# Kernel optimization log

Hardware: AMD Instinct MI355X
Metric: run time of the kernel (lower is better)

The kernel has to match this reference:

```python
import jax, jax.numpy as jnp
import numpy as np

B, S, HID = 1, 2048, 4096
NH, NKV = 32, 8
HD = HID // NH            # 128
GROUPS = NH // NKV        # 4
ROPE_THETA = 10000.0


def _rope_cos_sin(seq_len, head_dim, dtype=jnp.float32):
    inv_freq = 1.0 / (ROPE_THETA ** (jnp.arange(0, head_dim, 2, dtype=jnp.float32) / head_dim))
    t = jnp.arange(seq_len, dtype=jnp.float32)
    freqs = jnp.outer(t, inv_freq)                      # [S, HD/2]
    emb = jnp.concatenate([freqs, freqs], axis=-1)      # [S, HD]
    return jnp.cos(emb).astype(dtype), jnp.sin(emb).astype(dtype)


def _rotate_half(x):
    x1, x2 = jnp.split(x, 2, axis=-1)
    return jnp.concatenate([-x2, x1], axis=-1)


def _apply_rope(x, cos, sin):
    # x: [B, H, S, HD]; cos/sin: [S, HD] (position_ids = arange(S), no past)
    return x * cos[None, None] + _rotate_half(x) * sin[None, None]


def setup_inputs() -> dict:
    key = jax.random.key(0)
    k1, k2, k3, k4, k5 = jax.random.split(key, 5)
    return {
        "hidden_states": jax.random.normal(k1, (B, S, HID), jnp.float32),
        "Wq": jax.random.normal(k2, (NH * HD, HID), jnp.float32) * 0.02,
        "Wk": jax.random.normal(k3, (NKV * HD, HID), jnp.float32) * 0.02,
        "Wv": jax.random.normal(k4, (NKV * HD, HID), jnp.float32) * 0.02,
        "Wo": jax.random.normal(k5, (HID, NH * HD), jnp.float32) * 0.02,
    }


def reference(hidden_states, Wq, Wk, Wv, Wo):
    bsz, q_len, _ = hidden_states.shape
    # projections (nn.Linear: x @ W.T)
    q = (hidden_states @ Wq.T).reshape(bsz, q_len, NH, HD).transpose(0, 2, 1, 3)   # [B,NH,S,HD]
    k = (hidden_states @ Wk.T).reshape(bsz, q_len, NKV, HD).transpose(0, 2, 1, 3)  # [B,NKV,S,HD]
    v = (hidden_states @ Wv.T).reshape(bsz, q_len, NKV, HD).transpose(0, 2, 1, 3)

    cos, sin = _rope_cos_sin(q_len, HD, hidden_states.dtype)
    q = _apply_rope(q, cos, sin)
    k = _apply_rope(k, cos, sin)

    # GQA: repeat kv heads (repeat_kv / num_key_value_groups)
    k = jnp.repeat(k, GROUPS, axis=1)   # [B,NH,S,HD]
    v = jnp.repeat(v, GROUPS, axis=1)

    scale = 1.0 / jnp.sqrt(jnp.asarray(HD, hidden_states.dtype))
    logits = jnp.einsum('bhqd,bhkd->bhqk', q, k) * scale   # [B,NH,S,S]

    # prefill causal mask (phys_past_len = 0)
    causal = jnp.tril(jnp.ones((q_len, q_len), dtype=bool))
    logits = jnp.where(causal[None, None], logits, jnp.finfo(logits.dtype).min)

    attn = jax.nn.softmax(logits, axis=-1)
    out = jnp.einsum('bhqk,bhkd->bhqd', attn, v)            # [B,NH,S,HD]
    out = out.transpose(0, 2, 1, 3).reshape(bsz, q_len, NH * HD)
    return out @ Wo.T
```

## Files before the change

### kernel.cpp

```cpp
#include <hip/hip_runtime.h>

typedef __bf16 bf16;
typedef __bf16 bf16x2 __attribute__((ext_vector_type(2)));
typedef __bf16 bf16x4 __attribute__((ext_vector_type(4)));
typedef __bf16 bf16x8 __attribute__((ext_vector_type(8)));
typedef float f32x4 __attribute__((ext_vector_type(4)));

#define S_LEN 2048
#define HID_DIM 4096
#define NH 32
#define NKV 8
#define HD 128
#define QKV_N 6144
#define K_COL 4096
#define V_COL 5120
#define PADV 76

__global__ void cvt_all_kernel(const float* __restrict__ hs, const float* __restrict__ wq,
                               const float* __restrict__ wk, const float* __restrict__ wv,
                               const float* __restrict__ wo, bf16* __restrict__ hsb,
                               bf16* __restrict__ wqkvb, bf16* __restrict__ wob,
                               float* __restrict__ cost, float* __restrict__ sint) {
  long i = (long)blockIdx.x * blockDim.x + threadIdx.x;
  if (i >= 12582912) {
    int j = (int)(i - 12582912);
    int s = j >> 6, d = j & 63;
    float inv = expf(-0.14391156831212787f * (float)d);
    float ang = (float)s * inv;
    cost[j] = cosf(ang);
    sint[j] = sinf(ang);
    return;
  }
  const float* src; bf16* dst; long off;
  if (i < 2097152)      { src = hs; dst = hsb;                          off = i; }
  else if (i < 6291456) { src = wq; dst = wqkvb;                        off = i - 2097152; }
  else if (i < 7340032) { src = wk; dst = wqkvb + (long)4096 * 4096;    off = i - 6291456; }
  else if (i < 8388608) { src = wv; dst = wqkvb + (long)5120 * 4096;    off = i - 7340032; }
  else                  { src = wo; dst = wob;                          off = i - 8388608; }
  float4 v = reinterpret_cast<const float4*>(src)[off];
  bf16x4 o;
  o[0] = (bf16)v.x; o[1] = (bf16)v.y; o[2] = (bf16)v.z; o[3] = (bf16)v.w;
  reinterpret_cast<bf16x4*>(dst)[off] = o;
}

__global__ void rope_apply_kernel(bf16* __restrict__ qkv, const float* __restrict__ cost,
                                  const float* __restrict__ sint) {
  int idx = blockIdx.x * blockDim.x + threadIdx.x;
  int s = idx / 320;
  int c = idx - s * 320;
  int g = c >> 3, dc = (c & 7) * 8;
  long base = (long)s * QKV_N + g * 128 + dc;
  bf16x8 x1 = *reinterpret_cast<const bf16x8*>(qkv + base);
  bf16x8 x2 = *reinterpret_cast<const bf16x8*>(qkv + base + 64);
  const float* cp = cost + (s << 6) + dc;
  const float* sp = sint + (s << 6) + dc;
  float4 ca = *reinterpret_cast<const float4*>(cp);
  float4 cb = *reinterpret_cast<const float4*>(cp + 4);
  float4 sa = *reinterpret_cast<const float4*>(sp);
  float4 sb = *reinterpret_cast<const float4*>(sp + 4);
  float co[8] = {ca.x, ca.y, ca.z, ca.w, cb.x, cb.y, cb.z, cb.w};
  float sn[8] = {sa.x, sa.y, sa.z, sa.w, sb.x, sb.y, sb.z, sb.w};
  bf16x8 y1, y2;
#pragma unroll
  for (int e = 0; e < 8; ++e) {
    float a = (float)x1[e], b = (float)x2[e];
    y1[e] = (bf16)(a * co[e] - b * sn[e]);
    y2[e] = (bf16)(b * co[e] + a * sn[e]);
  }
  *reinterpret_cast<bf16x8*>(qkv + base)      = y1;
  *reinterpret_cast<bf16x8*>(qkv + base + 64) = y2;
}

#define STG8(buf, mat, kt, unit) {                                                       \
    const bf16* sp_ = (mat) ? Bp : Ap;                                                   \
    int row0_ = ((mat) ? n0 : m0) + (unit) * 64;                                         \
    int lb_ = (buf) * LBUF + (mat) * 16384 + (unit) * 4096;                              \
    int r_ = t >> 3, jl_ = t & 7, jg_ = jl_ ^ (r_ & 7);                                  \
    const bf16* src_ = sp_ + (long)(row0_ + r_) * K + (kt) * 64 + jg_ * 8;               \
    __builtin_amdgcn_global_load_lds((const __attribute__((address_space(1))) void*)src_,\
        (__attribute__((address_space(3))) void*)(L + lb_ + t * 8), 16, 0, 0); }

#define DSA2(buf, mh) {                                                                  \
    _Pragma("unroll") for (int ks_ = 0; ks_ < 2; ++ks_)                                  \
      _Pragma("unroll") for (int mf_ = 0; mf_ < 4; ++mf_) {                              \
        int R_ = wr * 128 + (mh) * 64 + mf_ * 16 + lm;                                   \
        aF[ks_][mf_] = *reinterpret_cast<const bf16x8*>(                                 \
            L + (buf) * LBUF + R_ * 64 + (((ks_ * 4 + lg) ^ (R_ & 7)) << 3));            \
      } }

#define DSBALL(buf) {                                                                    \
    _Pragma("unroll") for (int ks_ = 0; ks_ < 2; ++ks_)                                  \
      _Pragma("unroll") for (int nf_ = 0; nf_ < NB; ++nf_) {                             \
        int R_ = wc * (NB * 16) + nf_ * 16 + lm;                                         \
        bF[ks_][nf_] = *reinterpret_cast<const bf16x8*>(                                 \
            L + (buf) * LBUF + 16384 + R_ * 64 + (((ks_ * 4 + lg) ^ (R_ & 7)) << 3));    \
      } }

#define MM2(mh) {                                                                        \
    __builtin_amdgcn_s_setprio(1);                                                       \
    _Pragma("unroll") for (int mf_ = 0; mf_ < 4; ++mf_)                                  \
      _Pragma("unroll") for (int nf_ = 0; nf_ < NB; ++nf_)                               \
        _Pragma("unroll") for (int ks_ = 0; ks_ < 2; ++ks_)                              \
          acc[(mh) * 4 + mf_][nf_] = __builtin_amdgcn_mfma_f32_16x16x32_bf16(            \
              aF[ks_][mf_], bF[ks_][nf_], acc[(mh) * 4 + mf_][nf_], 0, 0, 0);            \
    __builtin_amdgcn_s_setprio(0); }

#define BAR() __builtin_amdgcn_s_barrier()
#define WVM(n) asm volatile("s_waitcnt vmcnt(%0)" :: "i"(n) : "memory")

template<int NB, typename OutT>
__global__ __launch_bounds__(512, 1) void gemm4p_kernel(
    const bf16* __restrict__ Ap, const bf16* __restrict__ Bp, OutT* __restrict__ C,
    int M, int N, int K) {
  constexpr int LBUF = 16384 + NB * 4096;
  __shared__ __align__(16) bf16 L[2 * LBUF];

  int nwg = gridDim.x * gridDim.y;
  int bid = blockIdx.y * gridDim.x + blockIdx.x;
  int cpx = nwg >> 3;
  int swz = (bid & 7) * cpx + (bid >> 3);
  int bxs = swz % gridDim.x, bys = swz / gridDim.x;
  const int n0 = bxs * (NB * 64), m0 = bys * 256;

  const int t = threadIdx.x;
  const int lane = t & 63, w = t >> 6;
  const int wr = w >> 2, wc = w & 3;
  const int lg = lane >> 4, lm = lane & 15;
  const int NT = K >> 6;

  f32x4 acc[8][NB] = {};
  bf16x8 aF[2][4], bF[2][NB];

  STG8(0, 0, 0, 0); STG8(0, 0, 0, 1); STG8(0, 0, 0, 2); STG8(0, 0, 0, 3);
  STG8(0, 1, 0, 0); if (NB > 1) STG8(0, 1, 0, 1); if (NB > 2) STG8(0, 1, 0, 2);
  STG8(1, 1, 1, 0); if (NB > 1) STG8(1, 1, 1, 1); if (NB > 2) STG8(1, 1, 1, 2);
  WVM(NB);
  BAR();

  for (int I = 0; I < (NT >> 1); ++I) {
    const int tt = 2 * I;
    const bool pf = (I < (NT >> 1) - 1);
    DSA2(0, 0); DSBALL(0);
    STG8(1, 0, tt + 1, 0); STG8(1, 0, tt + 1, 1);
    STG8(1, 0, tt + 1, 2); STG8(1, 0, tt + 1, 3);
    BAR(); MM2(0); BAR();
    DSA2(0, 1);
    if (pf) { STG8(0, 1, tt + 2, 0); if (NB > 1) STG8(0, 1, tt + 2, 1);
              if (NB > 2) STG8(0, 1, tt + 2, 2); }
    BAR(); MM2(1);
    if (pf) WVM(NB); else WVM(0);
    BAR();
    DSA2(1, 0); DSBALL(1);
    if (pf) { STG8(0, 0, tt + 2, 0); STG8(0, 0, tt + 2, 1);
              STG8(0, 0, tt + 2, 2); STG8(0, 0, tt + 2, 3); }
    BAR(); MM2(0); BAR();
    DSA2(1, 1);
    if (pf) { STG8(1, 1, tt + 3, 0); if (NB > 1) STG8(1, 1, tt + 3, 1);
              if (NB > 2) STG8(1, 1, tt + 3, 2); }
    BAR(); MM2(1);
    if (pf) WVM(NB); else WVM(0);
    BAR();
  }

#pragma unroll
  for (int am = 0; am < 8; ++am) {
    int row = m0 + wr * 128 + am * 16 + lg * 4;
#pragma unroll
    for (int nf = 0; nf < NB; ++nf) {
      int col = n0 + wc * (NB * 16) + nf * 16 + lm;
#pragma unroll
      for (int rr = 0; rr < 4; ++rr) {
        if constexpr (sizeof(OutT) == 4) C[(long)(row + rr) * N + col] = acc[am][nf][rr];
        else                             C[(long)(row + rr) * N + col] = (bf16)acc[am][nf][rr];
      }
    }
  }
}

#define AK_LBAR() { asm volatile("s_waitcnt lgkmcnt(0)" ::: "memory");                   \
                    __builtin_amdgcn_s_barrier(); }
#define AK_VBAR() { asm volatile("s_waitcnt vmcnt(4)" ::: "memory");                     \
                    __builtin_amdgcn_sched_barrier(0);                                   \
                    asm volatile("s_waitcnt lgkmcnt(0)" ::: "memory");                   \
                    __builtin_amdgcn_s_barrier(); }

#define AK_WRITEV(r0, r1) {                                                              \
    _Pragma("unroll") for (int e = 0; e < 8; ++e) {                                      \
      bf16x2 pk; pk[0] = r0[e]; pk[1] = r1[e];                                           \
      *reinterpret_cast<bf16x2*>(Vt + (dchunk * 8 + e) * PADV + slot) = pk;              \
    } }

#define AK_ISSUEV(base, r0, r1) {                                                        \
    long rv_ = (long)(base) + kva; if (rv_ > 2046) rv_ = 2046;                           \
    const bf16* vs_ = vbase + rv_ * QKV_N + dchunk * 8;                                  \
    r0 = *reinterpret_cast<const bf16x8*>(vs_);                                          \
    r1 = *reinterpret_cast<const bf16x8*>(vs_ + QKV_N); }

#define AK_ISSUEK(base, buf) {                                                           \
    _Pragma("unroll") for (int i_ = 0; i_ < 2; ++i_) {                                   \
      int c_ = i_ * 512 + t;                                                             \
      int r_ = c_ >> 4, jl_ = c_ & 15, jg_ = jl_ ^ (r_ & 15);                            \
      long rk_ = (long)(base) + r_; if (rk_ > 2047) rk_ = 2047;                          \
      const bf16* src_ = kbase + rk_ * QKV_N + jg_ * 8;                                  \
      __builtin_amdgcn_global_load_lds((const __attribute__((address_space(1))) void*)src_,\
          (__attribute__((address_space(3))) void*)(Ks[buf] + c_ * 8), 16, 0, 0);        \
    } }

#define AK_STEP(stv, ksb) {                                                              \
    const int st_ = (stv);                                                               \
    const int kv0_ = st_ * 64;                                                           \
    if (kv0_ <= q0 + w * 16 + 15) {                                                      \
      f32x4 s[4];                                                                        \
      _Pragma("unroll") for (int cb = 0; cb < 4; ++cb) s[cb] = f32x4{0.f,0.f,0.f,0.f};   \
      __builtin_amdgcn_s_setprio(1);                                                     \
      _Pragma("unroll") for (int ks = 0; ks < 4; ++ks)                                   \
        _Pragma("unroll") for (int cb = 0; cb < 4; ++cb) {                               \
          bf16x8 kf = *reinterpret_cast<const bf16x8*>(                                  \
              Ks[ksb] + (cb * 16 + lm) * 128 + (((ks * 4 + lg) ^ lm) << 3));             \
          s[cb] = __builtin_amdgcn_mfma_f32_16x16x32_bf16(kf, qf[ks], s[cb], 0, 0, 0);   \
        }                                                                                \
      __builtin_amdgcn_s_setprio(0);                                                     \
      const float SC = 0.12751742f;                                                      \
      float sl[4][4];                                                                    \
      _Pragma("unroll") for (int cb = 0; cb < 4; ++cb)                                   \
        _Pragma("unroll") for (int r = 0; r < 4; ++r) {                                  \
          float v = s[cb][r] * SC;                                                       \
          if (st_ >= nst - 2 && (kv0_ + cb * 16 + lg * 4 + r) > qg) v = -1e30f;          \
          sl[cb][r] = v;                                                                 \
        }                                                                                \
      float tm = sl[0][0];                                                               \
      _Pragma("unroll") for (int cb = 0; cb < 4; ++cb)                                   \
        _Pragma("unroll") for (int r = 0; r < 4; ++r) tm = fmaxf(tm, sl[cb][r]);         \
      tm = fmaxf(tm, __shfl_xor(tm, 16));                                                \
      tm = fmaxf(tm, __shfl_xor(tm, 32));                                                \
      if (__any(tm > mrow + 8.f)) {                                                      \
        float mnew = fmaxf(mrow, tm);                                                    \
        float alpha = exp2f(mrow - mnew);                                                \
        mrow = mnew; lrow *= alpha;                                                      \
        float ar[4];                                                                     \
        _Pragma("unroll") for (int r = 0; r < 4; ++r)                                    \
          ar[r] = __shfl(alpha, (lane & 48) | (lg * 4 + r));                             \
        _Pragma("unroll") for (int i = 0; i < 8; ++i)                                    \
          _Pragma("unroll") for (int r = 0; r < 4; ++r) o[i][r] *= ar[r];                \
      }                                                                                  \
      float p[4][4]; float psum = 0.f;                                                   \
      _Pragma("unroll") for (int cb = 0; cb < 4; ++cb)                                   \
        _Pragma("unroll") for (int r = 0; r < 4; ++r) {                                  \
          p[cb][r] = exp2f(sl[cb][r] - mrow); psum += p[cb][r];                          \
        }                                                                                \
      psum += __shfl_xor(psum, 16);                                                      \
      psum += __shfl_xor(psum, 32);                                                      \
      lrow += psum;                                                                      \
      bf16x8 pa0, pa1;                                                                   \
      _Pragma("unroll") for (int r = 0; r < 4; ++r) {                                    \
        pa0[r] = (bf16)p[0][r]; pa0[4 + r] = (bf16)p[1][r];                              \
        pa1[r] = (bf16)p[2][r]; pa1[4 + r] = (bf16)p[3][r];                              \
      }                                                                                  \
      __builtin_amdgcn_s_setprio(1);                                                     \
      _Pragma("unroll") for (int db = 0; db < 8; ++db) {                                 \
        bf16x8 vf0 = *reinterpret_cast<const bf16x8*>(Vt + (db*16+lm)*PADV + lg*8);      \
        bf16x8 vf1 = *reinterpret_cast<const bf16x8*>(Vt + (db*16+lm)*PADV + 32 + lg*8); \
        o[db] = __builtin_amdgcn_mfma_f32_16x16x32_bf16(pa0, vf0, o[db], 0, 0, 0);       \
        o[db] = __builtin_amdgcn_mfma_f32_16x16x32_bf16(pa1, vf1, o[db], 0, 0, 0);       \
      }                                                                                  \
      __builtin_amdgcn_s_setprio(0);                                                     \
    } }

__global__ __launch_bounds__(512, 4) void attn_kernel(const bf16* __restrict__ qkv,
                                                      bf16* __restrict__ out) {
  __shared__ __align__(16) bf16 Ks[2][64 * 128];
  __shared__ __align__(16) bf16 Vt[128 * PADV];

  const int bx = blockIdx.x;
  const int qt = 15 - (bx >> 5);
  const int h = bx & 31;
  const int kvh = h >> 2;
  const int q0 = qt * 128;
  const int t = threadIdx.x, lane = t & 63, w = t >> 6;
  const int lg = lane >> 4, lm = lane & 15;
  const int dchunk = t >> 5, kv2 = t & 31;
  const int kva = kv2 * 2;
  const int k5 = kva & 31;
  const int slot = ((kva >> 5) << 5) | (((k5 >> 2) & 3) << 3) | ((k5 >> 4) << 2) | (k5 & 3);
  const bf16* kbase = qkv + K_COL + kvh * HD;
  const bf16* vbase = qkv + V_COL + kvh * HD;

  const long qrow = q0 + w * 16 + lm;
  const int qg = q0 + w * 16 + lm;
  bf16x8 qf[4];
#pragma unroll
  for (int ks = 0; ks < 4; ++ks)
    qf[ks] = *reinterpret_cast<const bf16x8*>(qkv + qrow * QKV_N + h * HD + ks * 32 + lg * 8);

  f32x4 o[8];
#pragma unroll
  for (int i = 0; i < 8; ++i) o[i] = f32x4{0.f, 0.f, 0.f, 0.f};
  float mrow = -1e30f, lrow = 0.f;

  const int nst = 2 * qt + 2;
  bf16x8 va0, va1, vb0, vb1;

  AK_ISSUEV(0, va0, va1);
  AK_ISSUEK(0, 0);
  AK_ISSUEV(64, vb0, vb1);
  AK_ISSUEK(64, 1);
  AK_WRITEV(va0, va1);
  AK_VBAR();

  for (int I = 0; I < (nst >> 1); ++I) {
    const int s0 = 2 * I;
    AK_STEP(s0, 0);
    AK_LBAR();
    AK_WRITEV(vb0, vb1);
    AK_ISSUEV((s0 + 2) * 64, va0, va1);
    AK_ISSUEK((s0 + 2) * 64, 0);
    AK_VBAR();
    AK_STEP(s0 + 1, 1);
    AK_LBAR();
    AK_WRITEV(va0, va1);
    AK_ISSUEV((s0 + 3) * 64, vb0, vb1);
    AK_ISSUEK((s0 + 3) * 64, 1);
    AK_VBAR();
  }

  float invr[4];
#pragma unroll
  for (int r = 0; r < 4; ++r)
    invr[r] = 1.0f / __shfl(lrow, (lane & 48) | (lg * 4 + r));
#pragma unroll
  for (int r = 0; r < 4; ++r) {
    long row = q0 + w * 16 + lg * 4 + r;
#pragma unroll
    for (int db = 0; db < 8; ++db)
      out[row * HID_DIM + h * HD + db * 16 + lm] = (bf16)(o[db][r] * invr[r]);
  }
}

extern "C" void kernel_launch(void* const* d_in, const int* in_sizes, int n_in,
                              void* d_out, int out_size, void* d_ws, size_t ws_size,
                              hipStream_t stream) {
  const float* hs = (const float*)d_in[0];
  const float* Wq = (const float*)d_in[1];
  const float* Wk = (const float*)d_in[2];
  const float* Wv = (const float*)d_in[3];
  const float* Wo = (const float*)d_in[4];
  float* out = (float*)d_out;
  char* ws = (char*)d_ws;

  bf16*  hsb   = (bf16*)(ws);
  bf16*  wqkvb = (bf16*)(ws + 16777216);
  bf16*  wob   = (bf16*)(ws + 67108864);
  bf16*  qkv   = (bf16*)(ws + 100663296);
  bf16*  attn  = (bf16*)(ws + 125829120);
  float* cost  = (float*)(ws + 142606336);
  float* sint  = (float*)(ws + 143130624);

  cvt_all_kernel<<<49664, 256, 0, stream>>>(hs, Wq, Wk, Wv, Wo, hsb, wqkvb, wob, cost, sint);
  gemm4p_kernel<3, bf16><<<dim3(32, 8), 512, 0, stream>>>(hsb, wqkvb, qkv, 2048, 6144, 4096);
  rope_apply_kernel<<<2560, 256, 0, stream>>>(qkv, cost, sint);
  attn_kernel<<<512, 512, 0, stream>>>(qkv, attn);
  gemm4p_kernel<2, float><<<dim3(32, 8), 512, 0, stream>>>(attn, wob, out, 2048, 4096, 4096);
}
```

Baseline: 302.5 us.

## Halve GEMM M-tile for more workgroups; double-buffer V in attention pipeline

```diff
diff --git a/kernel.cpp b/kernel.cpp
--- a/kernel.cpp
+++ b/kernel.cpp
@@ -71,48 +71,48 @@
   *reinterpret_cast<bf16x8*>(qkv + base + 64) = y2;
 }
 
-#define STG8(buf, mat, kt, unit) {                                                       \
+#define SG(buf, mat, kt, unit) {                                                         \
     const bf16* sp_ = (mat) ? Bp : Ap;                                                   \
     int row0_ = ((mat) ? n0 : m0) + (unit) * 64;                                         \
-    int lb_ = (buf) * LBUF + (mat) * 16384 + (unit) * 4096;                              \
+    int lb_ = (buf) * LBUF + (mat) * 8192 + (unit) * 4096;                               \
     int r_ = t >> 3, jl_ = t & 7, jg_ = jl_ ^ (r_ & 7);                                  \
     const bf16* src_ = sp_ + (long)(row0_ + r_) * K + (kt) * 64 + jg_ * 8;               \
     __builtin_amdgcn_global_load_lds((const __attribute__((address_space(1))) void*)src_,\
         (__attribute__((address_space(3))) void*)(L + lb_ + t * 8), 16, 0, 0); }
 
-#define DSA2(buf, mh) {                                                                  \
+#define RA(buf, mh) {                                                                    \
     _Pragma("unroll") for (int ks_ = 0; ks_ < 2; ++ks_)                                  \
-      _Pragma("unroll") for (int mf_ = 0; mf_ < 4; ++mf_) {                              \
-        int R_ = wr * 128 + (mh) * 64 + mf_ * 16 + lm;                                   \
+      _Pragma("unroll") for (int mf_ = 0; mf_ < 2; ++mf_) {                              \
+        int R_ = wr * 64 + (mh) * 32 + mf_ * 16 + lm;                                    \
         aF[ks_][mf_] = *reinterpret_cast<const bf16x8*>(                                 \
             L + (buf) * LBUF + R_ * 64 + (((ks_ * 4 + lg) ^ (R_ & 7)) << 3));            \
       } }
 
-#define DSBALL(buf) {                                                                    \
+#define RB(buf) {                                                                        \
     _Pragma("unroll") for (int ks_ = 0; ks_ < 2; ++ks_)                                  \
       _Pragma("unroll") for (int nf_ = 0; nf_ < NB; ++nf_) {                             \
         int R_ = wc * (NB * 16) + nf_ * 16 + lm;                                         \
         bF[ks_][nf_] = *reinterpret_cast<const bf16x8*>(                                 \
-            L + (buf) * LBUF + 16384 + R_ * 64 + (((ks_ * 4 + lg) ^ (R_ & 7)) << 3));    \
+            L + (buf) * LBUF + 8192 + R_ * 64 + (((ks_ * 4 + lg) ^ (R_ & 7)) << 3));     \
       } }
 
-#define MM2(mh) {                                                                        \
+#define MMH(mh) {                                                                        \
     __builtin_amdgcn_s_setprio(1);                                                       \
-    _Pragma("unroll") for (int mf_ = 0; mf_ < 4; ++mf_)                                  \
+    _Pragma("unroll") for (int mf_ = 0; mf_ < 2; ++mf_)                                  \
       _Pragma("unroll") for (int nf_ = 0; nf_ < NB; ++nf_)                               \
         _Pragma("unroll") for (int ks_ = 0; ks_ < 2; ++ks_)                              \
-          acc[(mh) * 4 + mf_][nf_] = __builtin_amdgcn_mfma_f32_16x16x32_bf16(            \
-              aF[ks_][mf_], bF[ks_][nf_], acc[(mh) * 4 + mf_][nf_], 0, 0, 0);            \
+          acc[(mh) * 2 + mf_][nf_] = __builtin_amdgcn_mfma_f32_16x16x32_bf16(            \
+              aF[ks_][mf_], bF[ks_][nf_], acc[(mh) * 2 + mf_][nf_], 0, 0, 0);            \
     __builtin_amdgcn_s_setprio(0); }
 
 #define BAR() __builtin_amdgcn_s_barrier()
 #define WVM(n) asm volatile("s_waitcnt vmcnt(%0)" :: "i"(n) : "memory")
 
 template<int NB, typename OutT>
-__global__ __launch_bounds__(512, 1) void gemm4p_kernel(
+__global__ __launch_bounds__(512, 4) void gemm4p_kernel(
     const bf16* __restrict__ Ap, const bf16* __restrict__ Bp, OutT* __restrict__ C,
     int M, int N, int K) {
-  constexpr int LBUF = 16384 + NB * 4096;
+  constexpr int LBUF = 8192 + NB * 4096;
   __shared__ __align__(16) bf16 L[2 * LBUF];
 
   int nwg = gridDim.x * gridDim.y;
@@ -120,7 +120,7 @@
   int cpx = nwg >> 3;
   int swz = (bid & 7) * cpx + (bid >> 3);
   int bxs = swz % gridDim.x, bys = swz / gridDim.x;
-  const int n0 = bxs * (NB * 64), m0 = bys * 256;
+  const int n0 = bxs * (NB * 64), m0 = bys * 128;
 
   const int t = threadIdx.x;
   const int lane = t & 63, w = t >> 6;
@@ -128,43 +128,41 @@
   const int lg = lane >> 4, lm = lane & 15;
   const int NT = K >> 6;
 
-  f32x4 acc[8][NB] = {};
-  bf16x8 aF[2][4], bF[2][NB];
-
-  STG8(0, 0, 0, 0); STG8(0, 0, 0, 1); STG8(0, 0, 0, 2); STG8(0, 0, 0, 3);
-  STG8(0, 1, 0, 0); if (NB > 1) STG8(0, 1, 0, 1); if (NB > 2) STG8(0, 1, 0, 2);
-  STG8(1, 1, 1, 0); if (NB > 1) STG8(1, 1, 1, 1); if (NB > 2) STG8(1, 1, 1, 2);
+  f32x4 acc[4][NB] = {};
+  bf16x8 aF[2][2], bF[2][NB];
+
+  SG(0, 0, 0, 0); SG(0, 0, 0, 1);
+  SG(0, 1, 0, 0); if (NB > 1) SG(0, 1, 0, 1); if (NB > 2) SG(0, 1, 0, 2);
+  SG(1, 1, 1, 0); if (NB > 1) SG(1, 1, 1, 1); if (NB > 2) SG(1, 1, 1, 2);
   WVM(NB);
   BAR();
 
   for (int I = 0; I < (NT >> 1); ++I) {
     const int tt = 2 * I;
     const bool pf = (I < (NT >> 1) - 1);
-    DSA2(0, 0); DSBALL(0);
-    STG8(1, 0, tt + 1, 0); STG8(1, 0, tt + 1, 1);
-    STG8(1, 0, tt + 1, 2); STG8(1, 0, tt + 1, 3);
-    BAR(); MM2(0); BAR();
-    DSA2(0, 1);
-    if (pf) { STG8(0, 1, tt + 2, 0); if (NB > 1) STG8(0, 1, tt + 2, 1);
-              if (NB > 2) STG8(0, 1, tt + 2, 2); }
-    BAR(); MM2(1);
+    RA(0, 0); RB(0);
+    SG(1, 0, tt + 1, 0); SG(1, 0, tt + 1, 1);
+    BAR(); MMH(0); BAR();
+    RA(0, 1);
+    if (pf) { SG(0, 1, tt + 2, 0); if (NB > 1) SG(0, 1, tt + 2, 1);
+              if (NB > 2) SG(0, 1, tt + 2, 2); }
+    BAR(); MMH(1);
     if (pf) WVM(NB); else WVM(0);
     BAR();
-    DSA2(1, 0); DSBALL(1);
-    if (pf) { STG8(0, 0, tt + 2, 0); STG8(0, 0, tt + 2, 1);
-              STG8(0, 0, tt + 2, 2); STG8(0, 0, tt + 2, 3); }
-    BAR(); MM2(0); BAR();
-    DSA2(1, 1);
-    if (pf) { STG8(1, 1, tt + 3, 0); if (NB > 1) STG8(1, 1, tt + 3, 1);
-              if (NB > 2) STG8(1, 1, tt + 3, 2); }
-    BAR(); MM2(1);
+    RA(1, 0); RB(1);
+    if (pf) { SG(0, 0, tt + 2, 0); SG(0, 0, tt + 2, 1); }
+    BAR(); MMH(0); BAR();
+    RA(1, 1);
+    if (pf) { SG(1, 1, tt + 3, 0); if (NB > 1) SG(1, 1, tt + 3, 1);
+              if (NB > 2) SG(1, 1, tt + 3, 2); }
+    BAR(); MMH(1);
     if (pf) WVM(NB); else WVM(0);
     BAR();
   }
 
 #pragma unroll
-  for (int am = 0; am < 8; ++am) {
-    int row = m0 + wr * 128 + am * 16 + lg * 4;
+  for (int am = 0; am < 4; ++am) {
+    int row = m0 + wr * 64 + am * 16 + lg * 4;
 #pragma unroll
     for (int nf = 0; nf < NB; ++nf) {
       int col = n0 + wc * (NB * 16) + nf * 16 + lm;
@@ -177,17 +175,15 @@
   }
 }
 
-#define AK_LBAR() { asm volatile("s_waitcnt lgkmcnt(0)" ::: "memory");                   \
-                    __builtin_amdgcn_s_barrier(); }
-#define AK_VBAR() { asm volatile("s_waitcnt vmcnt(4)" ::: "memory");                     \
-                    __builtin_amdgcn_sched_barrier(0);                                   \
-                    asm volatile("s_waitcnt lgkmcnt(0)" ::: "memory");                   \
-                    __builtin_amdgcn_s_barrier(); }
-
-#define AK_WRITEV(r0, r1) {                                                              \
+#define AK_BAR() { asm volatile("s_waitcnt vmcnt(2)" ::: "memory");                      \
+                   __builtin_amdgcn_sched_barrier(0);                                    \
+                   asm volatile("s_waitcnt lgkmcnt(0)" ::: "memory");                    \
+                   __builtin_amdgcn_s_barrier(); }
+
+#define AK_WRITEV(r0, r1, vtb) {                                                         \
     _Pragma("unroll") for (int e = 0; e < 8; ++e) {                                      \
       bf16x2 pk; pk[0] = r0[e]; pk[1] = r1[e];                                           \
-      *reinterpret_cast<bf16x2*>(Vt + (dchunk * 8 + e) * PADV + slot) = pk;              \
+      *reinterpret_cast<bf16x2*>(Vt[vtb] + (dchunk * 8 + e) * PADV + slot) = pk;         \
     } }
 
 #define AK_ISSUEV(base, r0, r1) {                                                        \
@@ -206,7 +202,7 @@
           (__attribute__((address_space(3))) void*)(Ks[buf] + c_ * 8), 16, 0, 0);        \
     } }
 
-#define AK_STEP(stv, ksb) {                                                              \
+#define AK_STEP(stv, bufb) {                                                             \
     const int st_ = (stv);                                                               \
     const int kv0_ = st_ * 64;                                                           \
     if (kv0_ <= q0 + w * 16 + 15) {                                                      \
@@ -216,7 +212,7 @@
       _Pragma("unroll") for (int ks = 0; ks < 4; ++ks)                                   \
         _Pragma("unroll") for (int cb = 0; cb < 4; ++cb) {                               \
           bf16x8 kf = *reinterpret_cast<const bf16x8*>(                                  \
-              Ks[ksb] + (cb * 16 + lm) * 128 + (((ks * 4 + lg) ^ lm) << 3));             \
+              Ks[bufb] + (cb * 16 + lm) * 128 + (((ks * 4 + lg) ^ lm) << 3));            \
           s[cb] = __builtin_amdgcn_mfma_f32_16x16x32_bf16(kf, qf[ks], s[cb], 0, 0, 0);   \
         }                                                                                \
       __builtin_amdgcn_s_setprio(0);                                                     \
@@ -258,8 +254,8 @@
       }                                                                                  \
       __builtin_amdgcn_s_setprio(1);                                                     \
       _Pragma("unroll") for (int db = 0; db < 8; ++db) {                                 \
-        bf16x8 vf0 = *reinterpret_cast<const bf16x8*>(Vt + (db*16+lm)*PADV + lg*8);      \
-        bf16x8 vf1 = *reinterpret_cast<const bf16x8*>(Vt + (db*16+lm)*PADV + 32 + lg*8); \
+        bf16x8 vf0 = *reinterpret_cast<const bf16x8*>(Vt[bufb] + (db*16+lm)*PADV + lg*8);\
+        bf16x8 vf1 = *reinterpret_cast<const bf16x8*>(Vt[bufb] + (db*16+lm)*PADV + 32 + lg*8);\
         o[db] = __builtin_amdgcn_mfma_f32_16x16x32_bf16(pa0, vf0, o[db], 0, 0, 0);       \
         o[db] = __builtin_amdgcn_mfma_f32_16x16x32_bf16(pa1, vf1, o[db], 0, 0, 0);       \
       }                                                                                  \
@@ -269,7 +265,7 @@
 __global__ __launch_bounds__(512, 4) void attn_kernel(const bf16* __restrict__ qkv,
                                                       bf16* __restrict__ out) {
   __shared__ __align__(16) bf16 Ks[2][64 * 128];
-  __shared__ __align__(16) bf16 Vt[128 * PADV];
+  __shared__ __align__(16) bf16 Vt[2][128 * PADV];
 
   const int bx = blockIdx.x;
   const int qt = 15 - (bx >> 5);
@@ -300,27 +296,25 @@
   const int nst = 2 * qt + 2;
   bf16x8 va0, va1, vb0, vb1;
 
+  AK_ISSUEK(0, 0);
   AK_ISSUEV(0, va0, va1);
-  AK_ISSUEK(0, 0);
+  AK_WRITEV(va0, va1, 0);
   AK_ISSUEV(64, vb0, vb1);
-  AK_ISSUEK(64, 1);
-  AK_WRITEV(va0, va1);
-  AK_VBAR();
+  asm volatile("s_waitcnt lgkmcnt(0)" ::: "memory");
+  __builtin_amdgcn_s_barrier();
 
   for (int I = 0; I < (nst >> 1); ++I) {
     const int s0 = 2 * I;
+    AK_ISSUEK((s0 + 1) * 64, 1);
+    AK_ISSUEV((s0 + 2) * 64, va0, va1);
+    AK_WRITEV(vb0, vb1, 1);
     AK_STEP(s0, 0);
-    AK_LBAR();
-    AK_WRITEV(vb0, vb1);
-    AK_ISSUEV((s0 + 2) * 64, va0, va1);
+    AK_BAR();
     AK_ISSUEK((s0 + 2) * 64, 0);
-    AK_VBAR();
+    AK_ISSUEV((s0 + 3) * 64, vb0, vb1);
+    AK_WRITEV(va0, va1, 0);
     AK_STEP(s0 + 1, 1);
-    AK_LBAR();
-    AK_WRITEV(va0, va1);
-    AK_ISSUEV((s0 + 3) * 64, vb0, vb1);
-    AK_ISSUEK((s0 + 3) * 64, 1);
-    AK_VBAR();
+    AK_BAR();
   }
 
   float invr[4];
@@ -356,8 +350,8 @@
   float* sint  = (float*)(ws + 143130624);
 
   cvt_all_kernel<<<49664, 256, 0, stream>>>(hs, Wq, Wk, Wv, Wo, hsb, wqkvb, wob, cost, sint);
-  gemm4p_kernel<3, bf16><<<dim3(32, 8), 512, 0, stream>>>(hsb, wqkvb, qkv, 2048, 6144, 4096);
+  gemm4p_kernel<3, bf16><<<dim3(32, 16), 512, 0, stream>>>(hsb, wqkvb, qkv, 2048, 6144, 4096);
   rope_apply_kernel<<<2560, 256, 0, stream>>>(qkv, cost, sint);
   attn_kernel<<<512, 512, 0, stream>>>(qkv, attn);
-  gemm4p_kernel<2, float><<<dim3(32, 8), 512, 0, stream>>>(attn, wob, out, 2048, 4096, 4096);
-}
+  gemm4p_kernel<2, float><<<dim3(32, 16), 512, 0, stream>>>(attn, wob, out, 2048, 4096, 4096);
+}
```

Measured after the change: 337.7 us. +11.6%, slower.
